# Kernel tuning notes

Hardware: AMD Instinct MI355X
Metric: run time of the kernel (lower is better)

Reference implementation:

```python
import jax, jax.numpy as jnp
import numpy as np

N_NODES = 50000
N_EDGES = 800000
NUM_FEATURES = 256
HIDDEN = 256
HEADS = 8
OUT_DIM = 2


def setup_inputs() -> dict:
    key = jax.random.key(0)
    ks = jax.random.split(key, 16)
    C1 = HIDDEN // HEADS  # 32 per-head channels
    inp = {
        'x': jax.random.normal(ks[0], (N_NODES, NUM_FEATURES), dtype=jnp.float32),
        'edge_index': jax.random.randint(ks[1], (2, N_EDGES), 0, N_NODES, dtype=jnp.int64),
        # layer 1: num_features -> heads * (hidden//heads)
        'W1': jax.random.normal(ks[2], (NUM_FEATURES, HEADS * C1), dtype=jnp.float32) * 0.05,
        'att_src1': jax.random.normal(ks[3], (HEADS, C1), dtype=jnp.float32) * 0.1,
        'att_dst1': jax.random.normal(ks[4], (HEADS, C1), dtype=jnp.float32) * 0.1,
        'b1': jnp.zeros((HEADS * C1,), dtype=jnp.float32),
        # layer 2: hidden -> heads * (hidden//heads)
        'W2': jax.random.normal(ks[5], (HIDDEN, HEADS * C1), dtype=jnp.float32) * 0.05,
        'att_src2': jax.random.normal(ks[6], (HEADS, C1), dtype=jnp.float32) * 0.1,
        'att_dst2': jax.random.normal(ks[7], (HEADS, C1), dtype=jnp.float32) * 0.1,
        'b2': jnp.zeros((HEADS * C1,), dtype=jnp.float32),
        # layer 3: hidden -> output_dim, heads=1, concat=False
        'W3': jax.random.normal(ks[8], (HIDDEN, OUT_DIM), dtype=jnp.float32) * 0.05,
        'att_src3': jax.random.normal(ks[9], (1, OUT_DIM), dtype=jnp.float32) * 0.1,
        'att_dst3': jax.random.normal(ks[10], (1, OUT_DIM), dtype=jnp.float32) * 0.1,
        'b3': jnp.zeros((OUT_DIM,), dtype=jnp.float32),
    }
    return inp


def _gat_layer(x, src, dst, W, a_src, a_dst, b, concat):
    # PyG GATConv: h = x W -> [N, H, C]; e_ij = leaky_relu(a_src.h_j + a_dst.h_i)
    # softmax over edges grouped by destination, then scatter-add h_j * alpha.
    N = x.shape[0]
    H, C = a_src.shape
    h = (x @ W).reshape(N, H, C)
    alpha_s = jnp.einsum('nhc,hc->nh', h, a_src)  # [N, H]
    alpha_d = jnp.einsum('nhc,hc->nh', h, a_dst)
    e = jax.nn.leaky_relu(alpha_s[src] + alpha_d[dst], negative_slope=0.2)  # [E, H]
    m = jax.ops.segment_max(e, dst, num_segments=N)  # per-dst max for stable softmax
    ee = jnp.exp(e - m[dst])
    denom = jax.ops.segment_sum(ee, dst, num_segments=N)
    alpha = ee / (denom[dst] + 1e-16)  # [E, H]
    msg = h[src] * alpha[:, :, None]  # [E, H, C]
    out = jax.ops.segment_sum(msg, dst, num_segments=N)  # [N, H, C]
    out = out.reshape(N, H * C) if concat else out.mean(axis=1)
    return out + b


def reference(x, edge_index, W1, att_src1, att_dst1, b1, W2, att_src2, att_dst2, b2, W3, att_src3, att_dst3, b3):
    N = x.shape[0]
    loops = jnp.arange(N, dtype=edge_index.dtype)
    src = jnp.concatenate([edge_index[0], loops])  # PyG add_self_loops=True
    dst = jnp.concatenate([edge_index[1], loops])
    h = _gat_layer(x, src, dst, W1, att_src1, att_dst1, b1, concat=True)
    h = jax.nn.elu(h)  # dropout is identity in eval mode
    h = _gat_layer(h, src, dst, W2, att_src2, att_dst2, b2, concat=True)
    h = jax.nn.elu(h)
    out = _gat_layer(h, src, dst, W3, att_src3, att_dst3, b3, concat=False)
    return out  # [N, output_dim]; batch=None so pooling/MLP head is skipped
```

## Files before the change

### kernel.cpp

```cpp
#include <hip/hip_runtime.h>
#include <math.h>

#define NF 256
#define NHEADS 8
#define MNEG -1e30f

typedef _Float16 half8 __attribute__((ext_vector_type(8)));
typedef float f32x4 __attribute__((ext_vector_type(4)));


__global__ __launch_bounds__(256) void deg_count_k(const int* __restrict__ dst, int* __restrict__ deg, int E) {
    int e = blockIdx.x * 256 + threadIdx.x;
    if (e < E) atomicAdd(&deg[dst[e]], 1);
}

__global__ __launch_bounds__(256) void scan1_k(const int* __restrict__ deg, int* __restrict__ indptr,
                                               int* __restrict__ bsum, int n) {
    __shared__ int sh[256];
    int tid = threadIdx.x;
    int i = blockIdx.x * 256 + tid;
    int d = (i < n) ? deg[i] : 0;
    sh[tid] = d;
    __syncthreads();
#pragma unroll
    for (int off = 1; off < 256; off <<= 1) {
        int t = (tid >= off) ? sh[tid - off] : 0;
        __syncthreads();
        sh[tid] += t;
        __syncthreads();
    }
    if (i < n) indptr[i] = sh[tid] - d;
    if (tid == 255) bsum[blockIdx.x] = sh[255];
}

__global__ __launch_bounds__(256) void scan3_k(const int* __restrict__ deg, int* __restrict__ indptr,
                                               const int* __restrict__ bsum, int* __restrict__ cursor,
                                               int* __restrict__ srcs, int n, int nb) {
    __shared__ int sh[256];
    int tid = threadIdx.x;
    int d = (tid < nb) ? bsum[tid] : 0;
    sh[tid] = d;
    __syncthreads();
#pragma unroll
    for (int off = 1; off < 256; off <<= 1) {
        int t = (tid >= off) ? sh[tid - off] : 0;
        __syncthreads();
        sh[tid] += t;
        __syncthreads();
    }
    int bid = blockIdx.x;
    int boff = sh[bid] - ((bid < nb) ? bsum[bid] : 0);
    int i = bid * 256 + tid;
    if (i < n) {
        int v = indptr[i] + boff + i;
        indptr[i] = v;
        srcs[v] = i;
        cursor[i] = v + 1;
        if (i == n - 1) indptr[n] = v + deg[i] + 1;
    }
}

__global__ __launch_bounds__(256) void fill_edge_k(const int* __restrict__ esrc, const int* __restrict__ edst,
                                                   int* __restrict__ cursor, int* __restrict__ srcs, int E) {
    int e = blockIdx.x * 256 + threadIdx.x;
    if (e < E) {
        int p = atomicAdd(&cursor[edst[e]], 1);
        srcs[p] = esrc[e];
    }
}


__global__ __launch_bounds__(256) void prep_w_k(const float* __restrict__ W1, const float* __restrict__ W2,
                                                _Float16* __restrict__ O1, _Float16* __restrict__ O2) {
    int tid = blockIdx.x * 256 + threadIdx.x;
    const float* W = (tid < 65536) ? W1 : W2;
    _Float16* O = (tid < 65536) ? O1 : O2;
    int t = tid & 65535;
    int k = t >> 8, c = t & 255;
    O[(size_t)c * 256 + k] = (_Float16)W[t];
}


template <int AF32>
__global__ __launch_bounds__(512, 2) void gemm_mfma_k(const void* __restrict__ Av, const _Float16* __restrict__ WTh,
                                                      const float* __restrict__ att_s, const float* __restrict__ att_d,
                                                      _Float16* __restrict__ C, float* __restrict__ aS,
                                                      float* __restrict__ aD, int M) {
    __shared__ __align__(16) _Float16 WT[256][264];
    int t = threadIdx.x;
#pragma unroll
    for (int it = 0; it < 16; ++it) {
        int col = it * 16 + (t >> 5);
        int kc = (t & 31) * 8;
        *(half8*)&WT[col][kc] = *(const half8*)&WTh[(size_t)col * 256 + kc];
    }
    __syncthreads();

    int wave = t >> 6, lane = t & 63;
    int wm = wave >> 2, wn = wave & 3;
    int lr = lane & 15, lg = lane >> 4;
    int r0 = blockIdx.x * 256 + wm * 128;
    int c0 = wn * 64;
    const float* Af = (const float*)Av;
    const _Float16* Ah = (const _Float16*)Av;

    f32x4 acc[8][4];
#pragma unroll
    for (int mr = 0; mr < 8; ++mr)
#pragma unroll
        for (int nr = 0; nr < 4; ++nr) acc[mr][nr] = (f32x4){0.f, 0.f, 0.f, 0.f};

    for (int ks = 0; ks < 8; ++ks) {
        int k0 = ks * 32;
        half8 a[8];
#pragma unroll
        for (int mr = 0; mr < 8; ++mr) {
            int row = r0 + mr * 16 + lr;
            row = row < M ? row : M - 1;
            if (AF32) {
                const float* p = Af + (size_t)row * 256 + k0 + lg * 8;
                float4 x0 = *(const float4*)p;
                float4 x1 = *(const float4*)(p + 4);
                half8 av;
                av[0] = (_Float16)x0.x; av[1] = (_Float16)x0.y; av[2] = (_Float16)x0.z; av[3] = (_Float16)x0.w;
                av[4] = (_Float16)x1.x; av[5] = (_Float16)x1.y; av[6] = (_Float16)x1.z; av[7] = (_Float16)x1.w;
                a[mr] = av;
            } else {
                a[mr] = *(const half8*)(Ah + (size_t)row * 256 + k0 + lg * 8);
            }
        }
        half8 b[4];
#pragma unroll
        for (int nr = 0; nr < 4; ++nr)
            b[nr] = *(const half8*)&WT[c0 + nr * 16 + lr][k0 + lg * 8];
#pragma unroll
        for (int mr = 0; mr < 8; ++mr)
#pragma unroll
            for (int nr = 0; nr < 4; ++nr)
                acc[mr][nr] = __builtin_amdgcn_mfma_f32_16x16x32_f16(a[mr], b[nr], acc[mr][nr], 0, 0, 0);
    }

    int h0 = wn * 2, h1 = wn * 2 + 1;
    float as_c0 = att_s[h0 * 32 + lr],      as_c1 = att_s[h0 * 32 + 16 + lr];
    float as_c2 = att_s[h1 * 32 + lr],      as_c3 = att_s[h1 * 32 + 16 + lr];
    float ad_c0 = att_d[h0 * 32 + lr],      ad_c1 = att_d[h0 * 32 + 16 + lr];
    float ad_c2 = att_d[h1 * 32 + lr],      ad_c3 = att_d[h1 * 32 + 16 + lr];

#pragma unroll
    for (int mr = 0; mr < 8; ++mr) {
        int rbase = r0 + mr * 16 + lg * 4;
#pragma unroll
        for (int j = 0; j < 4; ++j) {
            int row = rbase + j;
            float ps0 = acc[mr][0][j] * as_c0 + acc[mr][1][j] * as_c1;
            float ps1 = acc[mr][2][j] * as_c2 + acc[mr][3][j] * as_c3;
            float pd0 = acc[mr][0][j] * ad_c0 + acc[mr][1][j] * ad_c1;
            float pd1 = acc[mr][2][j] * ad_c2 + acc[mr][3][j] * ad_c3;
#pragma unroll
            for (int o = 1; o < 16; o <<= 1) {
                ps0 += __shfl_xor(ps0, o);
                ps1 += __shfl_xor(ps1, o);
                pd0 += __shfl_xor(pd0, o);
                pd1 += __shfl_xor(pd1, o);
            }
            if (row < M) {
#pragma unroll
                for (int nr = 0; nr < 4; ++nr)
                    C[(size_t)row * 256 + c0 + nr * 16 + lr] = (_Float16)acc[mr][nr][j];
                if (lr == 0) {
                    aS[(size_t)row * NHEADS + h0] = ps0;
                    aS[(size_t)row * NHEADS + h1] = ps1;
                    aD[(size_t)row * NHEADS + h0] = pd0;
                    aD[(size_t)row * NHEADS + h1] = pd1;
                }
            }
        }
    }
}


template <int MODE>
__global__ __launch_bounds__(256) void agg_k(const _Float16* __restrict__ h, const float* __restrict__ aS,
                                             const float* __restrict__ aD, const int* __restrict__ indptr,
                                             const int* __restrict__ srcs, const float* __restrict__ bias,
                                             _Float16* __restrict__ out,
                                             const float* __restrict__ W3, const float* __restrict__ as3,
                                             const float* __restrict__ ad3, float* __restrict__ h3,
                                             float* __restrict__ s3, float* __restrict__ d3, int N) {
    int wid = blockIdx.x * 4 + (threadIdx.x >> 6);
    if (wid >= N) return;
    int lane = threadIdx.x & 63;
    int hf = lane >> 5;
    int cl = lane & 31;
    int hh = cl >> 2;
    float ad = aD[(size_t)wid * NHEADS + hh];
    int beg = indptr[wid], end = indptr[wid + 1];
    const half8* h8p = (const half8*)h;
    float m = MNEG, den = 0.f;
    float f0 = 0, f1 = 0, f2 = 0, f3 = 0, f4 = 0, f5 = 0, f6 = 0, f7 = 0;
    int k = beg;
    int sp[4];
    if (k + 8 <= end) {
#pragma unroll
        for (int j = 0; j < 4; ++j) sp[j] = srcs[k + 2 * j + hf];
    }
    for (; k + 8 <= end; k += 8) {
        int s[4]; float as[4]; half8 v[4]; float e[4];
#pragma unroll
        for (int j = 0; j < 4; ++j) s[j] = sp[j];
        if (k + 16 <= end) {
#pragma unroll
            for (int j = 0; j < 4; ++j) sp[j] = srcs[k + 8 + 2 * j + hf];
        }
#pragma unroll
        for (int j = 0; j < 4; ++j) as[j] = aS[(size_t)s[j] * NHEADS + hh];
#pragma unroll
        for (int j = 0; j < 4; ++j) v[j] = h8p[(size_t)s[j] * 32 + cl];
#pragma unroll
        for (int j = 0; j < 4; ++j) { e[j] = as[j] + ad; e[j] = fmaxf(e[j], 0.2f * e[j]); }
        float em = fmaxf(fmaxf(e[0], e[1]), fmaxf(e[2], e[3]));
        if (__any(em > m + 4.f)) {
            float mn = fmaxf(m, em);
            float sc = __expf(m - mn);
            den *= sc; f0 *= sc; f1 *= sc; f2 *= sc; f3 *= sc; f4 *= sc; f5 *= sc; f6 *= sc; f7 *= sc;
            m = mn;
        }
        half8 hacc = (half8)(_Float16)0.f;
#pragma unroll
        for (int j = 0; j < 4; ++j) {
            float p = __expf(e[j] - m);
            den += p;
            _Float16 ph = (_Float16)p;
            half8 pb = {ph, ph, ph, ph, ph, ph, ph, ph};
            hacc += v[j] * pb;
        }
        f0 += (float)hacc[0]; f1 += (float)hacc[1]; f2 += (float)hacc[2]; f3 += (float)hacc[3];
        f4 += (float)hacc[4]; f5 += (float)hacc[5]; f6 += (float)hacc[6]; f7 += (float)hacc[7];
    }
    for (; k + 2 <= end; k += 2) {
        int s = srcs[k + hf];
        float as = aS[(size_t)s * NHEADS + hh];
        half8 v = h8p[(size_t)s * 32 + cl];
        float e = as + ad; e = fmaxf(e, 0.2f * e);
        if (__any(e > m + 4.f)) {
            float mn = fmaxf(m, e);
            float sc = __expf(m - mn);
            den *= sc; f0 *= sc; f1 *= sc; f2 *= sc; f3 *= sc; f4 *= sc; f5 *= sc; f6 *= sc; f7 *= sc;
            m = mn;
        }
        float p = __expf(e - m);
        den += p;
        f0 += p * (float)v[0]; f1 += p * (float)v[1]; f2 += p * (float)v[2]; f3 += p * (float)v[3];
        f4 += p * (float)v[4]; f5 += p * (float)v[5]; f6 += p * (float)v[6]; f7 += p * (float)v[7];
    }
    if (k < end) {
        int s = srcs[k];
        float e = aS[(size_t)s * NHEADS + hh] + ad;
        e = fmaxf(e, 0.2f * e);
        half8 v = h8p[(size_t)s * 32 + cl];
        float eg = (hf == 0) ? e : MNEG;
        if (__any(eg > m + 4.f)) {
            float mn = fmaxf(m, eg);
            float sc = __expf(m - mn);
            den *= sc; f0 *= sc; f1 *= sc; f2 *= sc; f3 *= sc; f4 *= sc; f5 *= sc; f6 *= sc; f7 *= sc;
            m = mn;
        }
        float p = (hf == 0) ? __expf(e - m) : 0.f;
        den += p;
        f0 += p * (float)v[0]; f1 += p * (float)v[1]; f2 += p * (float)v[2]; f3 += p * (float)v[3];
        f4 += p * (float)v[4]; f5 += p * (float)v[5]; f6 += p * (float)v[6]; f7 += p * (float)v[7];
    }
    {
        float m2 = __shfl_xor(m, 32);
        float den2 = __shfl_xor(den, 32);
        float mn = fmaxf(m, m2);
        float sc1 = __expf(m - mn), sc2 = __expf(m2 - mn);
        den = den * sc1 + den2 * sc2;
        f0 = f0 * sc1 + __shfl_xor(f0, 32) * sc2;
        f1 = f1 * sc1 + __shfl_xor(f1, 32) * sc2;
        f2 = f2 * sc1 + __shfl_xor(f2, 32) * sc2;
        f3 = f3 * sc1 + __shfl_xor(f3, 32) * sc2;
        f4 = f4 * sc1 + __shfl_xor(f4, 32) * sc2;
        f5 = f5 * sc1 + __shfl_xor(f5, 32) * sc2;
        f6 = f6 * sc1 + __shfl_xor(f6, 32) * sc2;
        f7 = f7 * sc1 + __shfl_xor(f7, 32) * sc2;
    }
    float inv = 1.f / (den + 1e-16f);
    float4 bv0 = *(const float4*)&bias[cl * 8];
    float4 bv1 = *(const float4*)&bias[cl * 8 + 4];
    float o[8];
    o[0] = f0 * inv + bv0.x; o[1] = f1 * inv + bv0.y; o[2] = f2 * inv + bv0.z; o[3] = f3 * inv + bv0.w;
    o[4] = f4 * inv + bv1.x; o[5] = f5 * inv + bv1.y; o[6] = f6 * inv + bv1.z; o[7] = f7 * inv + bv1.w;
#pragma unroll
    for (int c = 0; c < 8; ++c) o[c] = (o[c] > 0.f) ? o[c] : expm1f(o[c]);

    if (MODE == 0) {
        if (hf == 0) {
            half8 ov;
#pragma unroll
            for (int c = 0; c < 8; ++c) ov[c] = (_Float16)o[c];
            ((half8*)out)[(size_t)wid * 32 + cl] = ov;
        }
    } else {
        const float4* W34 = (const float4*)W3;
        float p0 = 0.f, p1 = 0.f;
#pragma unroll
        for (int q = 0; q < 4; ++q) {
            float4 w = W34[cl * 4 + q];
            p0 += o[2 * q] * w.x + o[2 * q + 1] * w.z;
            p1 += o[2 * q] * w.y + o[2 * q + 1] * w.w;
        }
#pragma unroll
        for (int off = 1; off < 32; off <<= 1) {
            p0 += __shfl_xor(p0, off);
            p1 += __shfl_xor(p1, off);
        }
        if (lane == 0) {
            h3[(size_t)wid * 2] = p0;
            h3[(size_t)wid * 2 + 1] = p1;
            s3[wid] = p0 * as3[0] + p1 * as3[1];
            d3[wid] = p0 * ad3[0] + p1 * ad3[1];
        }
    }
}


__global__ __launch_bounds__(256) void agg3_k(const float* __restrict__ h3, const float* __restrict__ s3,
                                              const float* __restrict__ d3, const int* __restrict__ indptr,
                                              const int* __restrict__ srcs, const float* __restrict__ b3,
                                              float* __restrict__ out, int N) {
    int t = blockIdx.x * 256 + threadIdx.x;
    int n = t >> 2;
    if (n >= N) return;
    int sub = t & 3;
    float ad = d3[n];
    float m = MNEG, den = 0.f, a0 = 0.f, a1 = 0.f;
    int beg = indptr[n], end = indptr[n + 1];
    for (int k = beg + sub; k < end; k += 4) {
        int s = srcs[k];
        float e = s3[s] + ad;
        e = fmaxf(e, 0.2f * e);
        if (e > m + 8.f) {
            float mn = fmaxf(m, e);
            float sc = __expf(m - mn);
            den *= sc; a0 *= sc; a1 *= sc;
            m = mn;
        }
        float p = __expf(e - m);
        den += p;
        a0 += p * h3[(size_t)s * 2];
        a1 += p * h3[(size_t)s * 2 + 1];
    }
#pragma unroll
    for (int off = 1; off < 4; off <<= 1) {
        float m2 = __shfl_xor(m, off);
        float den2 = __shfl_xor(den, off);
        float a02 = __shfl_xor(a0, off);
        float a12 = __shfl_xor(a1, off);
        float mn = fmaxf(m, m2);
        float sc1 = __expf(m - mn);
        float sc2 = __expf(m2 - mn);
        den = den * sc1 + den2 * sc2;
        a0 = a0 * sc1 + a02 * sc2;
        a1 = a1 * sc1 + a12 * sc2;
        m = mn;
    }
    if (sub == 0) {
        float inv = 1.f / (den + 1e-16f);
        out[(size_t)n * 2]     = a0 * inv + b3[0];
        out[(size_t)n * 2 + 1] = a1 * inv + b3[1];
    }
}


extern "C" void kernel_launch(void* const* d_in, const int* in_sizes, int n_in,
                              void* d_out, int out_size, void* d_ws, size_t ws_size,
                              hipStream_t stream) {
    const float* x   = (const float*)d_in[0];
    const int*   ei  = (const int*)d_in[1];
    const float* W1  = (const float*)d_in[2];
    const float* as1 = (const float*)d_in[3];
    const float* ad1 = (const float*)d_in[4];
    const float* b1  = (const float*)d_in[5];
    const float* W2  = (const float*)d_in[6];
    const float* as2 = (const float*)d_in[7];
    const float* ad2 = (const float*)d_in[8];
    const float* b2  = (const float*)d_in[9];
    const float* W3  = (const float*)d_in[10];
    const float* at_s3 = (const float*)d_in[11];
    const float* at_d3 = (const float*)d_in[12];
    const float* b3  = (const float*)d_in[13];

    int N = in_sizes[0] / NF;
    int E = in_sizes[1] / 2;
    const int* esrc = ei;
    const int* edst = ei + E;

    char* w = (char*)d_ws;
    _Float16* hbuf  = (_Float16*)w; w += (size_t)N * NF * 2;
    _Float16* xnext = (_Float16*)w; w += (size_t)N * NF * 2;
    float* aS    = (float*)w; w += (size_t)N * NHEADS * 4;
    float* aD    = (float*)w; w += (size_t)N * NHEADS * 4;
    float* h3    = (float*)w; w += (size_t)N * 2 * 4;
    float* s3    = (float*)w; w += (size_t)N * 4;
    float* d3    = (float*)w; w += (size_t)N * 4;
    int* deg     = (int*)w; w += (size_t)N * 4;
    int* indptr  = (int*)w; w += (size_t)(N + 1) * 4 + 60;
    int* cursor  = (int*)w; w += (size_t)N * 4;
    int* bsum    = (int*)w; w += 256 * 4;
    _Float16* WTh1 = (_Float16*)w; w += (size_t)256 * 256 * 2;
    _Float16* WTh2 = (_Float16*)w; w += (size_t)256 * 256 * 2;
    int* srcs    = (int*)w;

    int nb_n = (N + 255) / 256;
    int nb_e = (E + 255) / 256;
    int nb_w = (N + 3) / 4;
    int nb_g = (N + 255) / 256;
    int nb_a3 = (N * 4 + 255) / 256;

    hipMemsetAsync(deg, 0, (size_t)N * 4, stream);
    deg_count_k<<<nb_e, 256, 0, stream>>>(edst, deg, E);
    scan1_k<<<nb_n, 256, 0, stream>>>(deg, indptr, bsum, N);
    scan3_k<<<nb_n, 256, 0, stream>>>(deg, indptr, bsum, cursor, srcs, N, nb_n);
    fill_edge_k<<<nb_e, 256, 0, stream>>>(esrc, edst, cursor, srcs, E);
    prep_w_k<<<512, 256, 0, stream>>>(W1, W2, WTh1, WTh2);

    gemm_mfma_k<1><<<nb_g, 512, 0, stream>>>(x, WTh1, as1, ad1, hbuf, aS, aD, N);
    agg_k<0><<<nb_w, 256, 0, stream>>>(hbuf, aS, aD, indptr, srcs, b1, xnext,
                                       nullptr, nullptr, nullptr, nullptr, nullptr, nullptr, N);
    gemm_mfma_k<0><<<nb_g, 512, 0, stream>>>(xnext, WTh2, as2, ad2, hbuf, aS, aD, N);
    agg_k<1><<<nb_w, 256, 0, stream>>>(hbuf, aS, aD, indptr, srcs, b2, nullptr,
                                       W3, at_s3, at_d3, h3, s3, d3, N);
    agg3_k<<<nb_a3, 256, 0, stream>>>(h3, s3, d3, indptr, srcs, b3, (float*)d_out, N);
}
```

Baseline: 328.5 us.

## Restructure GEMM into K-chunked shared-memory tiles with smaller row blocks

The fused projection GEMM previously loaded the whole 256x256 transposed weight into LDS (~135KB) and had each wave read A rows straight from global memory. It now stages 64-wide K chunks of both A (128 rows) and W into LDS, halves the rows per block to 128, and shrinks the accumulator array. The goal is a much smaller LDS footprint and fewer registers so more blocks fit per CU (launch bounds raised to 4) and A reads are coalesced and shared. The cost is an extra sync per K step and W being re-read from global/L2 by each of twice as many blocks, with no double buffering to hide load latency.

```diff
diff --git a/kernel.cpp b/kernel.cpp
--- a/kernel.cpp
+++ b/kernel.cpp
@@ -82,64 +82,79 @@
 
 
 template <int AF32>
-__global__ __launch_bounds__(512, 2) void gemm_mfma_k(const void* __restrict__ Av, const _Float16* __restrict__ WTh,
+__global__ __launch_bounds__(512, 4) void gemm_mfma_k(const void* __restrict__ Av, const _Float16* __restrict__ WTh,
                                                       const float* __restrict__ att_s, const float* __restrict__ att_d,
                                                       _Float16* __restrict__ C, float* __restrict__ aS,
                                                       float* __restrict__ aD, int M) {
-    __shared__ __align__(16) _Float16 WT[256][264];
+    __shared__ __align__(16) _Float16 Asub[128][72];
+    __shared__ __align__(16) _Float16 Wsub[256][72];
     int t = threadIdx.x;
-#pragma unroll
-    for (int it = 0; it < 16; ++it) {
-        int col = it * 16 + (t >> 5);
-        int kc = (t & 31) * 8;
-        *(half8*)&WT[col][kc] = *(const half8*)&WTh[(size_t)col * 256 + kc];
-    }
-    __syncthreads();
-
     int wave = t >> 6, lane = t & 63;
     int wm = wave >> 2, wn = wave & 3;
     int lr = lane & 15, lg = lane >> 4;
-    int r0 = blockIdx.x * 256 + wm * 128;
-    int c0 = wn * 64;
+    int r0 = blockIdx.x * 128;
     const float* Af = (const float*)Av;
     const _Float16* Ah = (const _Float16*)Av;
 
-    f32x4 acc[8][4];
-#pragma unroll
-    for (int mr = 0; mr < 8; ++mr)
+    int arow = t >> 2;
+    int akoff = (t & 3) * 16;
+    int wcol = t >> 1;
+    int wkoff = (t & 1) * 32;
+    int ga_row = r0 + arow; ga_row = ga_row < M ? ga_row : M - 1;
+
+    f32x4 acc[4][4];
+#pragma unroll
+    for (int mr = 0; mr < 4; ++mr)
 #pragma unroll
         for (int nr = 0; nr < 4; ++nr) acc[mr][nr] = (f32x4){0.f, 0.f, 0.f, 0.f};
 
-    for (int ks = 0; ks < 8; ++ks) {
-        int k0 = ks * 32;
-        half8 a[8];
-#pragma unroll
-        for (int mr = 0; mr < 8; ++mr) {
-            int row = r0 + mr * 16 + lr;
-            row = row < M ? row : M - 1;
-            if (AF32) {
-                const float* p = Af + (size_t)row * 256 + k0 + lg * 8;
-                float4 x0 = *(const float4*)p;
-                float4 x1 = *(const float4*)(p + 4);
-                half8 av;
-                av[0] = (_Float16)x0.x; av[1] = (_Float16)x0.y; av[2] = (_Float16)x0.z; av[3] = (_Float16)x0.w;
-                av[4] = (_Float16)x1.x; av[5] = (_Float16)x1.y; av[6] = (_Float16)x1.z; av[7] = (_Float16)x1.w;
-                a[mr] = av;
-            } else {
-                a[mr] = *(const half8*)(Ah + (size_t)row * 256 + k0 + lg * 8);
-            }
-        }
-        half8 b[4];
-#pragma unroll
-        for (int nr = 0; nr < 4; ++nr)
-            b[nr] = *(const half8*)&WT[c0 + nr * 16 + lr][k0 + lg * 8];
-#pragma unroll
-        for (int mr = 0; mr < 8; ++mr)
+    for (int ks = 0; ks < 4; ++ks) {
+        int k0 = ks * 64;
+        __syncthreads();
+        if (AF32) {
+            const float* p = Af + (size_t)ga_row * 256 + k0 + akoff;
+            float4 x0 = *(const float4*)p;
+            float4 x1 = *(const float4*)(p + 4);
+            float4 x2 = *(const float4*)(p + 8);
+            float4 x3 = *(const float4*)(p + 12);
+            half8 h0, h1;
+            h0[0] = (_Float16)x0.x; h0[1] = (_Float16)x0.y; h0[2] = (_Float16)x0.z; h0[3] = (_Float16)x0.w;
+            h0[4] = (_Float16)x1.x; h0[5] = (_Float16)x1.y; h0[6] = (_Float16)x1.z; h0[7] = (_Float16)x1.w;
+            h1[0] = (_Float16)x2.x; h1[1] = (_Float16)x2.y; h1[2] = (_Float16)x2.z; h1[3] = (_Float16)x2.w;
+            h1[4] = (_Float16)x3.x; h1[5] = (_Float16)x3.y; h1[6] = (_Float16)x3.z; h1[7] = (_Float16)x3.w;
+            *(half8*)&Asub[arow][akoff] = h0;
+            *(half8*)&Asub[arow][akoff + 8] = h1;
+        } else {
+            const _Float16* p = Ah + (size_t)ga_row * 256 + k0 + akoff;
+            *(half8*)&Asub[arow][akoff] = *(const half8*)p;
+            *(half8*)&Asub[arow][akoff + 8] = *(const half8*)(p + 8);
+        }
+        {
+            const _Float16* p = WTh + (size_t)wcol * 256 + k0 + wkoff;
+            *(half8*)&Wsub[wcol][wkoff]      = *(const half8*)p;
+            *(half8*)&Wsub[wcol][wkoff + 8]  = *(const half8*)(p + 8);
+            *(half8*)&Wsub[wcol][wkoff + 16] = *(const half8*)(p + 16);
+            *(half8*)&Wsub[wcol][wkoff + 24] = *(const half8*)(p + 24);
+        }
+        __syncthreads();
+#pragma unroll
+        for (int kk = 0; kk < 2; ++kk) {
+            half8 a[4], b[4];
+#pragma unroll
+            for (int mr = 0; mr < 4; ++mr)
+                a[mr] = *(const half8*)&Asub[wm * 64 + mr * 16 + lr][kk * 32 + lg * 8];
 #pragma unroll
             for (int nr = 0; nr < 4; ++nr)
-                acc[mr][nr] = __builtin_amdgcn_mfma_f32_16x16x32_f16(a[mr], b[nr], acc[mr][nr], 0, 0, 0);
-    }
-
+                b[nr] = *(const half8*)&Wsub[wn * 64 + nr * 16 + lr][kk * 32 + lg * 8];
+#pragma unroll
+            for (int mr = 0; mr < 4; ++mr)
+#pragma unroll
+                for (int nr = 0; nr < 4; ++nr)
+                    acc[mr][nr] = __builtin_amdgcn_mfma_f32_16x16x32_f16(a[mr], b[nr], acc[mr][nr], 0, 0, 0);
+        }
+    }
+
+    int c0 = wn * 64;
     int h0 = wn * 2, h1 = wn * 2 + 1;
     float as_c0 = att_s[h0 * 32 + lr],      as_c1 = att_s[h0 * 32 + 16 + lr];
     float as_c2 = att_s[h1 * 32 + lr],      as_c3 = att_s[h1 * 32 + 16 + lr];
@@ -147,8 +162,8 @@
     float ad_c2 = att_d[h1 * 32 + lr],      ad_c3 = att_d[h1 * 32 + 16 + lr];
 
 #pragma unroll
-    for (int mr = 0; mr < 8; ++mr) {
-        int rbase = r0 + mr * 16 + lg * 4;
+    for (int mr = 0; mr < 4; ++mr) {
+        int rbase = r0 + wm * 64 + mr * 16 + lg * 4;
 #pragma unroll
         for (int j = 0; j < 4; ++j) {
             int row = rbase + j;
@@ -415,7 +430,7 @@
     int nb_n = (N + 255) / 256;
     int nb_e = (E + 255) / 256;
     int nb_w = (N + 3) / 4;
-    int nb_g = (N + 255) / 256;
+    int nb_gm = (N + 127) / 128;
     int nb_a3 = (N * 4 + 255) / 256;
 
     hipMemsetAsync(deg, 0, (size_t)N * 4, stream);
@@ -425,10 +440,10 @@
     fill_edge_k<<<nb_e, 256, 0, stream>>>(esrc, edst, cursor, srcs, E);
     prep_w_k<<<512, 256, 0, stream>>>(W1, W2, WTh1, WTh2);
 
-    gemm_mfma_k<1><<<nb_g, 512, 0, stream>>>(x, WTh1, as1, ad1, hbuf, aS, aD, N);
+    gemm_mfma_k<1><<<nb_gm, 512, 0, stream>>>(x, WTh1, as1, ad1, hbuf, aS, aD, N);
     agg_k<0><<<nb_w, 256, 0, stream>>>(hbuf, aS, aD, indptr, srcs, b1, xnext,
                                        nullptr, nullptr, nullptr, nullptr, nullptr, nullptr, N);
-    gemm_mfma_k<0><<<nb_g, 512, 0, stream>>>(xnext, WTh2, as2, ad2, hbuf, aS, aD, N);
+    gemm_mfma_k<0><<<nb_gm, 512, 0, stream>>>(xnext, WTh2, as2, ad2, hbuf, aS, aD, N);
     agg_k<1><<<nb_w, 256, 0, stream>>>(hbuf, aS, aD, indptr, srcs, b2, nullptr,
                                        W3, at_s3, at_d3, h3, s3, d3, N);
     agg3_k<<<nb_a3, 256, 0, stream>>>(h3, s3, d3, indptr, srcs, b3, (float*)d_out, N);
```

Result: faster. 300.7 us (-8.5%).
